# Optimization experiments

Measured on AMD Instinct MI355X. Metric: run time of the kernel, lower is better.

Reference implementation:

```python
import jax, jax.numpy as jnp
import numpy as np

NUM_LEVELS = 4
RADIUS = 4


def _bilinear_zeros(img, x, y):
    """Bilinear sample img (N,H,W) at absolute pixel coords x,y (N,S,S),
    zeros padding outside, matching torch grid_sample(align_corners=True,
    padding_mode='zeros') with absolute->normalized->absolute roundtrip."""
    N, H, W = img.shape
    x0 = jnp.floor(x); y0 = jnp.floor(y)
    x1 = x0 + 1.0;     y1 = y0 + 1.0
    wx1 = x - x0; wx0 = 1.0 - wx1
    wy1 = y - y0; wy0 = 1.0 - wy1
    flat = img.reshape(N, H * W)

    def gather(xi, yi):
        valid = (xi >= 0) & (xi <= W - 1) & (yi >= 0) & (yi <= H - 1)
        xc = jnp.clip(xi, 0, W - 1).astype(jnp.int32)
        yc = jnp.clip(yi, 0, H - 1).astype(jnp.int32)
        idx = (yc * W + xc).reshape(N, -1)
        v = jnp.take_along_axis(flat, idx, axis=1).reshape(xi.shape)
        return jnp.where(valid, v, jnp.zeros((), img.dtype))

    return (wy0 * wx0 * gather(x0, y0) + wy0 * wx1 * gather(x1, y0)
            + wy1 * wx0 * gather(x0, y1) + wy1 * wx1 * gather(x1, y1))


def _avg_pool2(v):
    N, H, W = v.shape
    return v.reshape(N, H // 2, 2, W // 2, 2).mean(axis=(2, 4))


def setup_inputs() -> dict:
    key = jax.random.key(0)
    k1, k2, k3 = jax.random.split(key, 3)
    B, M, C, H, W = 2, 4096, 256, 64, 64
    fmap1 = jax.random.normal(k1, (B, M, C), dtype=jnp.float32)
    fmap2 = jax.random.normal(k2, (B, C, H, W), dtype=jnp.float32)
    u = jax.random.uniform(k3, (B, M, 2), dtype=jnp.float32)
    centroids_coords = u * jnp.array([W - 1, H - 1], dtype=jnp.float32)
    return {"fmap1": fmap1, "fmap2": fmap2, "centroids_coords": centroids_coords}


def reference(fmap1, fmap2, centroids_coords):
    B, M, C = fmap1.shape
    _, _, H, W = fmap2.shape
    side = 2 * RADIUS + 1

    # correlation volume: (B, M, H, W) -> (B*M, H, W)
    corr = jnp.einsum('bmc,bchw->bmhw', fmap1, fmap2).reshape(B * M, H, W)

    d = jnp.arange(-RADIUS, RADIUS + 1, dtype=centroids_coords.dtype)
    di, dj = jnp.meshgrid(d, d, indexing='ij')
    delta = jnp.stack([di, dj], axis=-1)  # (S, S, 2): ch0 = x-offset, ch1 = y-offset

    c = centroids_coords.reshape(B * M, 1, 1, 2)
    vol = corr
    feats = []
    for lvl in range(NUM_LEVELS):
        sc = c + delta                        # (B*M, S, S, 2)
        sampled = _bilinear_zeros(vol, sc[..., 0], sc[..., 1])
        feats.append(sampled.reshape(B, M, side * side))
        c = c / 2.0
        if lvl < NUM_LEVELS - 1:
            vol = _avg_pool2(vol)
    # (B, M, num_levels*S*S) -> (B, out_channels, M)
    return jnp.concatenate(feats, axis=-1).transpose(0, 2, 1)
```

## Files before the change

### kernel.cpp

```cpp
#include <hip/hip_runtime.h>
#include <stdint.h>
#include <stddef.h>

static constexpr int Bb = 2;
static constexpr int Mq = 4096;
static constexpr int Cc = 256;
static constexpr int Hh = 64, Ww = 64;
static constexpr int Np = Hh * Ww;
static constexpr int NL1 = 1024;
static constexpr int RAD = 4;
static constexpr int SIDE = 2 * RAD + 1;
static constexpr int KPL = SIDE * SIDE;
static constexpr int NLVL = 4;
static constexpr int KTOT = NLVL * KPL;

static constexpr size_t WINBUF_B = 0;
static constexpr size_t ABF_B    = WINBUF_B + (size_t)Bb * Mq * 400 * 4;
static constexpr size_t BT_B     = ABF_B + (size_t)Bb * Mq * Cc * 2;
static constexpr size_t B1T_B    = BT_B + (size_t)Bb * Np * Cc * 2;
static constexpr size_t B2T_B    = B1T_B + (size_t)Bb * NL1 * Cc * 2;
static constexpr size_t B3T_B    = B2T_B + (size_t)Bb * 256 * Cc * 2;

typedef float floatx4 __attribute__((ext_vector_type(4)));
typedef short shortx8 __attribute__((ext_vector_type(8)));

union BfPack {
    shortx8 v;
    unsigned short u[8];
};

__device__ __forceinline__ unsigned short f2bf(float f) {
    unsigned int x = __float_as_uint(f);
    x += 0x7fffu + ((x >> 16) & 1u);
    return (unsigned short)(x >> 16);
}

__device__ __forceinline__ float bf2f(unsigned short u) {
    return __uint_as_float((unsigned int)u << 16);
}

__global__ __launch_bounds__(256)
void cvt_kernel(const float* __restrict__ f1, const float* __restrict__ f2,
                unsigned short* __restrict__ Abf, unsigned short* __restrict__ Bt,
                unsigned short* __restrict__ B1t)
{
    __shared__ float tile[64 * 132];
    const int tid = threadIdx.x;
    if (blockIdx.x < 1024) {
        const int t = blockIdx.x * 256 + tid;
        const float4 v0 = *(const float4*)(f1 + (size_t)t * 8);
        const float4 v1 = *(const float4*)(f1 + (size_t)t * 8 + 4);
        BfPack p;
        p.u[0] = f2bf(v0.x); p.u[1] = f2bf(v0.y);
        p.u[2] = f2bf(v0.z); p.u[3] = f2bf(v0.w);
        p.u[4] = f2bf(v1.x); p.u[5] = f2bf(v1.y);
        p.u[6] = f2bf(v1.z); p.u[7] = f2bf(v1.w);
        *(shortx8*)(Abf + (size_t)t * 8) = p.v;
        return;
    }
    const int bid  = blockIdx.x - 1024;
    const int b    = bid >> 7;
    const int cblk = (bid >> 5) & 3;
    const int y1   = bid & 31;

#pragma unroll
    for (int i = 0; i < 8; ++i) {
        const int v  = i * 256 + tid;
        const int c  = v >> 5;
        const int f4 = v & 31;
        *(float4*)&tile[c * 132 + f4 * 4] =
            *(const float4*)&f2[((size_t)(b * Cc + cblk * 64 + c)) * Np + y1 * 128 + f4 * 4];
    }
    __syncthreads();

#pragma unroll
    for (int i = 0; i < 4; ++i) {
        const int w  = i * 256 + tid;
        const int rp = w >> 3;
        const int cg = w & 7;
        BfPack p;
#pragma unroll
        for (int u = 0; u < 8; ++u)
            p.u[u] = f2bf(tile[(cg * 8 + u) * 132 + rp]);
        *(shortx8*)&Bt[((size_t)(b * Np + y1 * 128 + rp)) * Cc + cblk * 64 + cg * 8] = p.v;
    }

    {
        const int x1 = tid >> 3;
        const int cg = tid & 7;
        BfPack p;
#pragma unroll
        for (int u = 0; u < 8; ++u) {
            const int c = cg * 8 + u;
            const float v = 0.25f * (tile[c * 132 + 2 * x1]      + tile[c * 132 + 2 * x1 + 1]
                                   + tile[c * 132 + 64 + 2 * x1] + tile[c * 132 + 64 + 2 * x1 + 1]);
            p.u[u] = f2bf(v);
        }
        *(shortx8*)&B1t[((size_t)(b * NL1 + y1 * 32 + x1)) * Cc + cblk * 64 + cg * 8] = p.v;
    }
}

__global__ __launch_bounds__(256)
void pool23_kernel(const unsigned short* __restrict__ B1t,
                   unsigned short* __restrict__ B2t,
                   unsigned short* __restrict__ B3t)
{
    const int idx = blockIdx.x * 256 + threadIdx.x;
    if (idx < Bb * 256 * 32) {
        const int cg = idx & 31;
        const int p2 = (idx >> 5) & 255;
        const int b  = idx >> 13;
        const int y2 = p2 >> 4, x2 = p2 & 15;
        float s[8] = {0,0,0,0,0,0,0,0};
#pragma unroll
        for (int dy = 0; dy < 2; ++dy)
#pragma unroll
            for (int dx = 0; dx < 2; ++dx) {
                const int p1 = (2 * y2 + dy) * 32 + 2 * x2 + dx;
                BfPack v;
                v.v = *(const shortx8*)&B1t[((size_t)b * NL1 + p1) * Cc + cg * 8];
#pragma unroll
                for (int u = 0; u < 8; ++u) s[u] += bf2f(v.u[u]);
            }
        BfPack o;
#pragma unroll
        for (int u = 0; u < 8; ++u) o.u[u] = f2bf(0.25f * s[u]);
        *(shortx8*)&B2t[((size_t)b * 256 + p2) * Cc + cg * 8] = o.v;
    } else if (idx < Bb * 256 * 32 + Bb * 64 * 32) {
        const int i = idx - Bb * 256 * 32;
        const int cg = i & 31;
        const int p3 = (i >> 5) & 63;
        const int b  = i >> 11;
        const int y3 = p3 >> 3, x3 = p3 & 7;
        float s[8] = {0,0,0,0,0,0,0,0};
#pragma unroll
        for (int dy = 0; dy < 4; ++dy)
#pragma unroll
            for (int dx = 0; dx < 4; ++dx) {
                const int p1 = (4 * y3 + dy) * 32 + 4 * x3 + dx;
                BfPack v;
                v.v = *(const shortx8*)&B1t[((size_t)b * NL1 + p1) * Cc + cg * 8];
#pragma unroll
                for (int u = 0; u < 8; ++u) s[u] += bf2f(v.u[u]);
            }
        BfPack o;
#pragma unroll
        for (int u = 0; u < 8; ++u) o.u[u] = f2bf(0.0625f * s[u]);
        *(shortx8*)&B3t[((size_t)b * 64 + p3) * Cc + cg * 8] = o.v;
    }
}

__global__ __launch_bounds__(512)
void win4_kernel(const unsigned short* __restrict__ Abf,
                 const unsigned short* __restrict__ B0t,
                 const unsigned short* __restrict__ B1t,
                 const unsigned short* __restrict__ B2t,
                 const unsigned short* __restrict__ B3t,
                 const float* __restrict__ cent,
                 float* __restrict__ winbuf)
{
    __shared__ int qlist[128];
    __shared__ int qx0s[128], qy0s[128];
    __shared__ int qcnt;

    const int tid  = threadIdx.x;
    const int wave = tid >> 6;
    const int lane = tid & 63;
    const int lane15 = lane & 15;
    const int quad   = lane >> 4;
    const int bidx = blockIdx.x;

    int lvl, b, cell = 0, q0 = 0;
    bool binned;
    if (bidx < 512)      { lvl = 0; binned = true;  b = bidx >> 8;          cell = bidx & 255; }
    else if (bidx < 640) { lvl = 1; binned = true;  b = (bidx - 512) >> 6;  cell = (bidx - 512) & 63; }
    else if (bidx < 768) { lvl = 2; binned = false; b = (bidx - 640) >> 6;  q0 = ((bidx - 640) & 63) * 64; }
    else                 { lvl = 3; binned = false; b = (bidx - 768) >> 6;  q0 = ((bidx - 768) & 63) * 64; }

    const int w   = Ww >> lvl;
    const int npx = w * w;
    const float scale = 1.0f / (float)(1 << lvl);
    const unsigned short* Bl = (lvl == 0) ? B0t : (lvl == 1) ? B1t : (lvl == 2) ? B2t : B3t;

    int xmin = 0, ymin = 0, rh = w, rw = w, rstride = w, ntile = npx >> 4;
    int cnt;

    if (binned) {
        const int ncx  = w >> 2;
        const int binx = cell & (ncx - 1);
        const int biny = cell >> (4 - lvl);
        xmin = 4 * binx - 4; if (xmin < 0) xmin = 0;
        ymin = 4 * biny - 4; if (ymin < 0) ymin = 0;
        int xmax = 4 * binx + 8; if (xmax > w - 1) xmax = w - 1;
        int ymax = 4 * biny + 8; if (ymax > w - 1) ymax = w - 1;
        rh = ymax - ymin + 1; rw = xmax - xmin + 1;
        rstride = 13;
        ntile = (rh * 13 + 15) >> 4;

        if (tid == 0) qcnt = 0;
        __syncthreads();
#pragma unroll
        for (int i = 0; i < 8; ++i) {
            const int m = i * 512 + tid;
            const float2 cc = *(const float2*)&cent[((size_t)b * Mq + m) * 2];
            const int fx = (int)floorf(cc.x * scale);
            const int fy = (int)floorf(cc.y * scale);
            if ((fx >> 2) == binx && (fy >> 2) == biny) {
                const int idx = atomicAdd(&qcnt, 1);
                if (idx < 128) {
                    qlist[idx] = m;
                    qx0s[idx] = fx - RAD;
                    qy0s[idx] = fy - RAD;
                }
            }
        }
        __syncthreads();
        cnt = qcnt < 128 ? qcnt : 128;
    } else {
        if (tid < 64) {
            const int m = q0 + tid;
            const float2 cc = *(const float2*)&cent[((size_t)b * Mq + m) * 2];
            qlist[tid] = m;
            qx0s[tid] = (int)floorf(cc.x * scale) - RAD;
            qy0s[tid] = (int)floorf(cc.y * scale) - RAD;
        }
        __syncthreads();
        cnt = 64;
    }

    const int jt0 = wave, jt1 = wave + 8;
    const bool t0ok = jt0 < ntile;
    const bool t1ok = jt1 < ntile;
    int y0 = ymin, x0 = xmin, y1 = ymin, x1 = xmin;
    bool v0 = false, v1 = false;
    {
        const int px = jt0 * 16 + lane15;
        int py = (rstride == 13) ? ((px * 5043) >> 16) : (px >> (6 - lvl));
        const int pxx = px - py * rstride;
        v0 = t0ok && (py < rh) && (pxx < rw);
        if (py > rh - 1) py = rh - 1;
        const int pxc = pxx < rw ? pxx : rw - 1;
        y0 = ymin + py; x0 = xmin + pxc;
    }
    {
        const int px = jt1 * 16 + lane15;
        int py = (rstride == 13) ? ((px * 5043) >> 16) : (px >> (6 - lvl));
        const int pxx = px - py * rstride;
        v1 = t1ok && (py < rh) && (pxx < rw);
        if (py > rh - 1) py = rh - 1;
        const int pxc = pxx < rw ? pxx : rw - 1;
        y1 = ymin + py; x1 = xmin + pxc;
    }
    const size_t bB = (size_t)b * npx * Cc;
    const size_t off0 = bB + (size_t)(y0 * w + x0) * Cc + quad * 8;
    const size_t off1 = bB + (size_t)(y1 * w + x1) * Cc + quad * 8;

    for (int m0 = 0; m0 < cnt; m0 += 16) {
        const int qidx = (m0 + lane15) < cnt ? (m0 + lane15) : (cnt - 1);
        const unsigned short* arow = Abf + (size_t)(b * Mq + qlist[qidx]) * Cc + quad * 8;
        shortx8 afr[8];
#pragma unroll
        for (int k0 = 0; k0 < 8; ++k0)
            afr[k0] = *(const shortx8*)&arow[k0 * 32];

        floatx4 acc0 = {0.f, 0.f, 0.f, 0.f};
        floatx4 acc1 = {0.f, 0.f, 0.f, 0.f};
#pragma unroll
        for (int k0 = 0; k0 < 8; ++k0) {
            if (t0ok) {
                const shortx8 b0 = *(const shortx8*)&Bl[off0 + k0 * 32];
                acc0 = __builtin_amdgcn_mfma_f32_16x16x32_bf16(afr[k0], b0, acc0, 0, 0, 0);
            }
            if (t1ok) {
                const shortx8 b1 = *(const shortx8*)&Bl[off1 + k0 * 32];
                acc1 = __builtin_amdgcn_mfma_f32_16x16x32_bf16(afr[k0], b1, acc1, 0, 0, 0);
            }
        }

#pragma unroll
        for (int t = 0; t < 2; ++t) {
            const bool vv = (t == 0) ? v0 : v1;
            if (!vv) continue;
            const floatx4 a = (t == 0) ? acc0 : acc1;
            const int yy = (t == 0) ? y0 : y1;
            const int xx = (t == 0) ? x0 : x1;
#pragma unroll
            for (int r = 0; r < 4; ++r) {
                const int qi = m0 + quad * 4 + r;
                if (qi < cnt) {
                    const int wy = yy - qy0s[qi];
                    const int wx = xx - qx0s[qi];
                    if ((unsigned)wy < 10u && (unsigned)wx < 10u)
                        winbuf[((size_t)b * Mq + qlist[qi]) * 400 + lvl * 100 + wy * 10 + wx] = a[r];
                }
            }
        }
    }
}

__global__ __launch_bounds__(256)
void pyr_sample_kernel(const float* __restrict__ cent,
                       const float* __restrict__ winbuf,
                       float* __restrict__ out)
{
    __shared__ float win[8][400];
    __shared__ float qcx[8], qcy[8];
    __shared__ int qx0l[8][4], qy0l[8][4];

    const int tid = threadIdx.x;
    const int b   = blockIdx.x >> 9;
    const int m0  = (blockIdx.x & 511) * 8;
    const size_t gq0 = (size_t)(b * Mq + m0);

    if (tid < 32) {
        const int q = tid >> 2, l = tid & 3;
        const float cx = cent[(gq0 + q) * 2 + 0];
        const float cy = cent[(gq0 + q) * 2 + 1];
        if (l == 0) { qcx[q] = cx; qcy[q] = cy; }
        const float scl = 1.0f / (float)(1 << l);
        qx0l[q][l] = (int)floorf(cx * scl) - RAD;
        qy0l[q][l] = (int)floorf(cy * scl) - RAD;
    }
    for (int v = tid; v < 800; v += 256) {
        const int q = (v * 41) >> 12;
        const int o = v - q * 100;
        *(float4*)&win[q][o * 4] = *(const float4*)&winbuf[(gq0 + q) * 400 + o * 4];
    }
    __syncthreads();

    for (int i = 0; i < 11; ++i) {
        const int idx = i * 256 + tid;
        if (idx >= KTOT * 8) break;
        const int q  = idx & 7;
        const int kk = idx >> 3;
        const int lvl = kk / KPL;
        const int r   = kk - lvl * KPL;
        const int di  = r / SIDE;
        const int dj  = r - di * SIDE;

        const int w = Ww >> lvl;
        const float scale = 1.0f / (float)(1 << lvl);
        const float x = qcx[q] * scale + (float)(di - RAD);
        const float y = qcy[q] * scale + (float)(dj - RAD);

        const float x0f = floorf(x), y0f = floorf(y);
        const float wx1 = x - x0f, wx0 = 1.0f - wx1;
        const float wy1 = y - y0f, wy0 = 1.0f - wy1;
        const float fmx = (float)(w - 1);
        const bool vx0 = (x0f >= 0.0f) && (x0f <= fmx);
        const bool vx1 = (x0f + 1.0f >= 0.0f) && (x0f + 1.0f <= fmx);
        const bool vy0 = (y0f >= 0.0f) && (y0f <= fmx);
        const bool vy1 = (y0f + 1.0f >= 0.0f) && (y0f + 1.0f <= fmx);

        const int ix0 = (int)x0f, iy0 = (int)y0f;

        const float* buf = &win[q][lvl * 100];
        const int ox = qx0l[q][lvl], oy = qy0l[q][lvl];
        const int cx0 = ix0 - ox, cx1 = cx0 + 1;
        const int cy0r = iy0 - oy, cy1r = cy0r + 1;
        const float g00 = (vx0 && vy0) ? buf[cy0r * 10 + cx0] : 0.0f;
        const float g10 = (vx1 && vy0) ? buf[cy0r * 10 + cx1] : 0.0f;
        const float g01 = (vx0 && vy1) ? buf[cy1r * 10 + cx0] : 0.0f;
        const float g11 = (vx1 && vy1) ? buf[cy1r * 10 + cx1] : 0.0f;

        out[((size_t)b * KTOT + kk) * Mq + m0 + q] =
            wy0 * (wx0 * g00 + wx1 * g10) + wy1 * (wx0 * g01 + wx1 * g11);
    }
}

extern "C" void kernel_launch(void* const* d_in, const int* in_sizes, int n_in,
                              void* d_out, int out_size, void* d_ws, size_t ws_size,
                              hipStream_t stream)
{
    const float* fmap1 = (const float*)d_in[0];
    const float* fmap2 = (const float*)d_in[1];
    const float* cent  = (const float*)d_in[2];
    char* ws = (char*)d_ws;
    float* winbuf = (float*)(ws + WINBUF_B);
    unsigned short* Abf = (unsigned short*)(ws + ABF_B);
    unsigned short* Bt  = (unsigned short*)(ws + BT_B);
    unsigned short* B1t = (unsigned short*)(ws + B1T_B);
    unsigned short* B2t = (unsigned short*)(ws + B2T_B);
    unsigned short* B3t = (unsigned short*)(ws + B3T_B);
    float* out = (float*)d_out;

    cvt_kernel<<<1280, 256, 0, stream>>>(fmap1, fmap2, Abf, Bt, B1t);

    pool23_kernel<<<80, 256, 0, stream>>>(B1t, B2t, B3t);

    win4_kernel<<<896, 512, 0, stream>>>(Abf, Bt, B1t, B2t, B3t, cent, winbuf);

    pyr_sample_kernel<<<Bb * Mq / 8, 256, 0, stream>>>(cent, winbuf, out);
}
```

Baseline: 144.8 us.

## Fuse window correlation with bilinear sampling and prebin queries globally

Query binning moves into extra blocks of the conversion kernel, which use global atomics to build per-cell lists for every level. The window MFMA kernel is fused with the pyramid sampling kernel, so the 400-float per-query window buffer no longer makes a round trip through global memory and one launch is removed. B fragments are now held in registers and A rows are staged in LDS. Levels 2 and 3 now use spatial or index bins split into parts. The risks are list caps that can silently drop queries in dense cells and a new memset launch.

```diff
diff --git a/kernel.cpp b/kernel.cpp
--- a/kernel.cpp
+++ b/kernel.cpp
@@ -14,12 +14,13 @@
 static constexpr int NLVL = 4;
 static constexpr int KTOT = NLVL * KPL;
 
-static constexpr size_t WINBUF_B = 0;
-static constexpr size_t ABF_B    = WINBUF_B + (size_t)Bb * Mq * 400 * 4;
-static constexpr size_t BT_B     = ABF_B + (size_t)Bb * Mq * Cc * 2;
-static constexpr size_t B1T_B    = BT_B + (size_t)Bb * Np * Cc * 2;
-static constexpr size_t B2T_B    = B1T_B + (size_t)Bb * NL1 * Cc * 2;
-static constexpr size_t B3T_B    = B2T_B + (size_t)Bb * 256 * Cc * 2;
+static constexpr size_t ABF_B = 0;
+static constexpr size_t BT_B  = ABF_B + (size_t)Bb * Mq * Cc * 2;
+static constexpr size_t B1T_B = BT_B + (size_t)Bb * Np * Cc * 2;
+static constexpr size_t B2T_B = B1T_B + (size_t)Bb * NL1 * Cc * 2;
+static constexpr size_t B3T_B = B2T_B + (size_t)Bb * 256 * Cc * 2;
+static constexpr size_t CNT_B = B3T_B + (size_t)Bb * 64 * Cc * 2;
+static constexpr size_t LST_B = CNT_B + 4096;
 
 typedef float floatx4 __attribute__((ext_vector_type(4)));
 typedef short shortx8 __attribute__((ext_vector_type(8)));
@@ -41,8 +42,10 @@
 
 __global__ __launch_bounds__(256)
 void cvt_kernel(const float* __restrict__ f1, const float* __restrict__ f2,
+                const float* __restrict__ cent,
                 unsigned short* __restrict__ Abf, unsigned short* __restrict__ Bt,
-                unsigned short* __restrict__ B1t)
+                unsigned short* __restrict__ B1t,
+                int* __restrict__ cnts, int* __restrict__ lists)
 {
     __shared__ float tile[64 * 132];
     const int tid = threadIdx.x;
@@ -58,6 +61,41 @@
         *(shortx8*)(Abf + (size_t)t * 8) = p.v;
         return;
     }
+    if (blockIdx.x >= 1280) {
+        const int gq = (blockIdx.x - 1280) * 256 + tid;
+        const int b  = gq >> 12;
+        const int m  = gq & 4095;
+        const float2 cc = *(const float2*)&cent[(size_t)gq * 2];
+        {
+            const int fx = (int)floorf(cc.x);
+            const int fy = (int)floorf(cc.y);
+            const int cell = ((fy >> 2) << 4) | (fx >> 2);
+            const int slot = atomicAdd(&cnts[b * 256 + cell], 1);
+            if (slot < 64) lists[(b * 256 + cell) * 64 + slot] = m | (fx << 13) | (fy << 19);
+        }
+        {
+            const int fx = (int)floorf(cc.x * 0.5f);
+            const int fy = (int)floorf(cc.y * 0.5f);
+            const int cell = ((fy >> 2) << 3) | (fx >> 2);
+            const int slot = atomicAdd(&cnts[512 + b * 64 + cell], 1);
+            if (slot < 192) lists[32768 + (b * 64 + cell) * 192 + slot] = m | (fx << 13) | (fy << 19);
+        }
+        {
+            const int fx = (int)floorf(cc.x * 0.25f);
+            const int fy = (int)floorf(cc.y * 0.25f);
+            const int cell = ((fy >> 2) << 2) | (fx >> 2);
+            const int slot = atomicAdd(&cnts[640 + b * 16 + cell], 1);
+            if (slot < 512) lists[57344 + (b * 16 + cell) * 512 + slot] = m | (fx << 13) | (fy << 19);
+        }
+        {
+            const int fx = (int)floorf(cc.x * 0.125f);
+            const int fy = (int)floorf(cc.y * 0.125f);
+            const int cell = m >> 8;
+            const int slot = atomicAdd(&cnts[672 + b * 16 + cell], 1);
+            if (slot < 256) lists[73728 + (b * 16 + cell) * 256 + slot] = m | (fx << 13) | (fy << 19);
+        }
+        return;
+    }
     const int bid  = blockIdx.x - 1024;
     const int b    = bid >> 7;
     const int cblk = (bid >> 5) & 3;
@@ -151,220 +189,188 @@
 }
 
 __global__ __launch_bounds__(512)
-void win4_kernel(const unsigned short* __restrict__ Abf,
-                 const unsigned short* __restrict__ B0t,
-                 const unsigned short* __restrict__ B1t,
-                 const unsigned short* __restrict__ B2t,
-                 const unsigned short* __restrict__ B3t,
-                 const float* __restrict__ cent,
-                 float* __restrict__ winbuf)
+void win4f_kernel(const unsigned short* __restrict__ Abf,
+                  const unsigned short* __restrict__ B0t,
+                  const unsigned short* __restrict__ B1t,
+                  const unsigned short* __restrict__ B2t,
+                  const unsigned short* __restrict__ B3t,
+                  const float* __restrict__ cent,
+                  const int* __restrict__ cnts,
+                  const int* __restrict__ lists,
+                  float* __restrict__ out)
 {
-    __shared__ int qlist[128];
-    __shared__ int qx0s[128], qy0s[128];
-    __shared__ int qcnt;
-
-    const int tid  = threadIdx.x;
-    const int wave = tid >> 6;
-    const int lane = tid & 63;
+    __shared__ unsigned short Alds[16 * 264];
+    __shared__ float win[16][100];
+    __shared__ int llist[128];
+    __shared__ float qcx[16], qcy[16];
+    __shared__ int qx0c[16], qy0c[16];
+
+    const int tid    = threadIdx.x;
+    const int wave   = tid >> 6;
+    const int lane   = tid & 63;
     const int lane15 = lane & 15;
     const int quad   = lane >> 4;
-    const int bidx = blockIdx.x;
-
-    int lvl, b, cell = 0, q0 = 0;
-    bool binned;
-    if (bidx < 512)      { lvl = 0; binned = true;  b = bidx >> 8;          cell = bidx & 255; }
-    else if (bidx < 640) { lvl = 1; binned = true;  b = (bidx - 512) >> 6;  cell = (bidx - 512) & 63; }
-    else if (bidx < 768) { lvl = 2; binned = false; b = (bidx - 640) >> 6;  q0 = ((bidx - 640) & 63) * 64; }
-    else                 { lvl = 3; binned = false; b = (bidx - 768) >> 6;  q0 = ((bidx - 768) & 63) * 64; }
+    const int bx     = blockIdx.x;
+
+    int lvl, b, cell, part, plog, cap, cbase, lbase;
+    if (bx < 512)      { lvl = 0; b = bx >> 8; cell = bx & 255; part = 0; plog = 0; cap = 64;
+                         cbase = b * 256 + cell;        lbase = (b * 256 + cell) * 64; }
+    else if (bx < 768) { lvl = 1; const int u = bx - 512; b = u >> 7; const int c = u & 127;
+                         cell = c >> 1; part = c & 1; plog = 1; cap = 192;
+                         cbase = 512 + b * 64 + cell;   lbase = 32768 + (b * 64 + cell) * 192; }
+    else if (bx < 896) { lvl = 2; const int u = bx - 768; b = u >> 6; const int c = u & 63;
+                         cell = c >> 2; part = c & 3; plog = 2; cap = 512;
+                         cbase = 640 + b * 16 + cell;   lbase = 57344 + (b * 16 + cell) * 512; }
+    else               { lvl = 3; const int u = bx - 896; b = u >> 6; const int c = u & 63;
+                         cell = c >> 2; part = c & 3; plog = 2; cap = 256;
+                         cbase = 672 + b * 16 + cell;   lbase = 73728 + (b * 16 + cell) * 256; }
 
     const int w   = Ww >> lvl;
     const int npx = w * w;
     const float scale = 1.0f / (float)(1 << lvl);
     const unsigned short* Bl = (lvl == 0) ? B0t : (lvl == 1) ? B1t : (lvl == 2) ? B2t : B3t;
 
-    int xmin = 0, ymin = 0, rh = w, rw = w, rstride = w, ntile = npx >> 4;
-    int cnt;
-
-    if (binned) {
-        const int ncx  = w >> 2;
-        const int binx = cell & (ncx - 1);
-        const int biny = cell >> (4 - lvl);
+    int cnt = cnts[cbase]; if (cnt > cap) cnt = cap;
+    const int psz = (cnt + (1 << plog) - 1) >> plog;
+    const int p0 = part * psz;
+    int p1 = p0 + psz; if (p1 > cnt) p1 = cnt;
+    const int nloc = p1 - p0;
+    if (nloc <= 0) return;
+
+    int xmin = 0, ymin = 0, rh = w, rw = w;
+    if (lvl < 3) {
+        const int ncxl = 4 - lvl;
+        const int binx = cell & ((1 << ncxl) - 1);
+        const int biny = cell >> ncxl;
         xmin = 4 * binx - 4; if (xmin < 0) xmin = 0;
         ymin = 4 * biny - 4; if (ymin < 0) ymin = 0;
         int xmax = 4 * binx + 8; if (xmax > w - 1) xmax = w - 1;
         int ymax = 4 * biny + 8; if (ymax > w - 1) ymax = w - 1;
         rh = ymax - ymin + 1; rw = xmax - xmin + 1;
-        rstride = 13;
-        ntile = (rh * 13 + 15) >> 4;
-
-        if (tid == 0) qcnt = 0;
-        __syncthreads();
-#pragma unroll
-        for (int i = 0; i < 8; ++i) {
-            const int m = i * 512 + tid;
-            const float2 cc = *(const float2*)&cent[((size_t)b * Mq + m) * 2];
-            const int fx = (int)floorf(cc.x * scale);
-            const int fy = (int)floorf(cc.y * scale);
-            if ((fx >> 2) == binx && (fy >> 2) == biny) {
-                const int idx = atomicAdd(&qcnt, 1);
-                if (idx < 128) {
-                    qlist[idx] = m;
-                    qx0s[idx] = fx - RAD;
-                    qy0s[idx] = fy - RAD;
-                }
-            }
-        }
-        __syncthreads();
-        cnt = qcnt < 128 ? qcnt : 128;
-    } else {
-        if (tid < 64) {
-            const int m = q0 + tid;
-            const float2 cc = *(const float2*)&cent[((size_t)b * Mq + m) * 2];
-            qlist[tid] = m;
-            qx0s[tid] = (int)floorf(cc.x * scale) - RAD;
-            qy0s[tid] = (int)floorf(cc.y * scale) - RAD;
-        }
-        __syncthreads();
-        cnt = 64;
-    }
-
+    }
+
+    if (tid < nloc) llist[tid] = lists[lbase + p0 + tid];
+
+    const int ntile = ((rh - 1) * 13 + rw + 15) >> 4;
     const int jt0 = wave, jt1 = wave + 8;
     const bool t0ok = jt0 < ntile;
     const bool t1ok = jt1 < ntile;
-    int y0 = ymin, x0 = xmin, y1 = ymin, x1 = xmin;
+    int y0 = ymin, x0p = xmin, y1 = ymin, x1p = xmin;
     bool v0 = false, v1 = false;
     {
-        const int px = jt0 * 16 + lane15;
-        int py = (rstride == 13) ? ((px * 5043) >> 16) : (px >> (6 - lvl));
-        const int pxx = px - py * rstride;
+        const int px  = jt0 * 16 + lane15;
+        const int py  = (px * 5043) >> 16;
+        const int pxx = px - py * 13;
         v0 = t0ok && (py < rh) && (pxx < rw);
-        if (py > rh - 1) py = rh - 1;
-        const int pxc = pxx < rw ? pxx : rw - 1;
-        y0 = ymin + py; x0 = xmin + pxc;
+        y0  = ymin + (py < rh ? py : rh - 1);
+        x0p = xmin + (pxx < rw ? pxx : rw - 1);
     }
     {
-        const int px = jt1 * 16 + lane15;
-        int py = (rstride == 13) ? ((px * 5043) >> 16) : (px >> (6 - lvl));
-        const int pxx = px - py * rstride;
+        const int px  = jt1 * 16 + lane15;
+        const int py  = (px * 5043) >> 16;
+        const int pxx = px - py * 13;
         v1 = t1ok && (py < rh) && (pxx < rw);
-        if (py > rh - 1) py = rh - 1;
-        const int pxc = pxx < rw ? pxx : rw - 1;
-        y1 = ymin + py; x1 = xmin + pxc;
-    }
-    const size_t bB = (size_t)b * npx * Cc;
-    const size_t off0 = bB + (size_t)(y0 * w + x0) * Cc + quad * 8;
-    const size_t off1 = bB + (size_t)(y1 * w + x1) * Cc + quad * 8;
-
-    for (int m0 = 0; m0 < cnt; m0 += 16) {
-        const int qidx = (m0 + lane15) < cnt ? (m0 + lane15) : (cnt - 1);
-        const unsigned short* arow = Abf + (size_t)(b * Mq + qlist[qidx]) * Cc + quad * 8;
-        shortx8 afr[8];
-#pragma unroll
-        for (int k0 = 0; k0 < 8; ++k0)
-            afr[k0] = *(const shortx8*)&arow[k0 * 32];
+        y1  = ymin + (py < rh ? py : rh - 1);
+        x1p = xmin + (pxx < rw ? pxx : rw - 1);
+    }
+    const unsigned short* bsrc = Bl + (size_t)b * npx * Cc;
+    const unsigned short* bp0 = bsrc + (size_t)(y0 * w + x0p) * Cc + quad * 8;
+    const unsigned short* bp1 = bsrc + (size_t)(y1 * w + x1p) * Cc + quad * 8;
+    shortx8 bfr0[8], bfr1[8];
+#pragma unroll
+    for (int k0 = 0; k0 < 8; ++k0) bfr0[k0] = *(const shortx8*)&bp0[k0 * 32];
+#pragma unroll
+    for (int k0 = 0; k0 < 8; ++k0) bfr1[k0] = *(const shortx8*)&bp1[k0 * 32];
+
+    for (int m0 = 0; m0 < nloc; m0 += 16) {
+        __syncthreads();
+        {
+            const int r  = tid >> 5;
+            const int kc = tid & 31;
+            const int gi = m0 + r;
+            const int e  = llist[gi < nloc ? gi : nloc - 1];
+            const int m  = e & 8191;
+            *(shortx8*)&Alds[r * 264 + kc * 8] =
+                *(const shortx8*)&Abf[((size_t)(b * Mq) + m) * Cc + kc * 8];
+            if (tid < 16) {
+                const int gi2 = m0 + tid;
+                const int e2  = llist[gi2 < nloc ? gi2 : nloc - 1];
+                const int m2  = e2 & 8191;
+                const float2 cc = *(const float2*)&cent[((size_t)(b * Mq) + m2) * 2];
+                qcx[tid] = cc.x; qcy[tid] = cc.y;
+                qx0c[tid] = ((e2 >> 13) & 63) - RAD;
+                qy0c[tid] = ((e2 >> 19) & 63) - RAD;
+            }
+        }
+        __syncthreads();
 
         floatx4 acc0 = {0.f, 0.f, 0.f, 0.f};
         floatx4 acc1 = {0.f, 0.f, 0.f, 0.f};
 #pragma unroll
         for (int k0 = 0; k0 < 8; ++k0) {
-            if (t0ok) {
-                const shortx8 b0 = *(const shortx8*)&Bl[off0 + k0 * 32];
-                acc0 = __builtin_amdgcn_mfma_f32_16x16x32_bf16(afr[k0], b0, acc0, 0, 0, 0);
-            }
-            if (t1ok) {
-                const shortx8 b1 = *(const shortx8*)&Bl[off1 + k0 * 32];
-                acc1 = __builtin_amdgcn_mfma_f32_16x16x32_bf16(afr[k0], b1, acc1, 0, 0, 0);
-            }
+            const shortx8 a = *(const shortx8*)&Alds[lane15 * 264 + k0 * 32 + quad * 8];
+            if (t0ok) acc0 = __builtin_amdgcn_mfma_f32_16x16x32_bf16(a, bfr0[k0], acc0, 0, 0, 0);
+            if (t1ok) acc1 = __builtin_amdgcn_mfma_f32_16x16x32_bf16(a, bfr1[k0], acc1, 0, 0, 0);
         }
 
 #pragma unroll
         for (int t = 0; t < 2; ++t) {
             const bool vv = (t == 0) ? v0 : v1;
             if (!vv) continue;
-            const floatx4 a = (t == 0) ? acc0 : acc1;
+            const floatx4 aa = (t == 0) ? acc0 : acc1;
             const int yy = (t == 0) ? y0 : y1;
-            const int xx = (t == 0) ? x0 : x1;
+            const int xx = (t == 0) ? x0p : x1p;
 #pragma unroll
             for (int r = 0; r < 4; ++r) {
-                const int qi = m0 + quad * 4 + r;
-                if (qi < cnt) {
-                    const int wy = yy - qy0s[qi];
-                    const int wx = xx - qx0s[qi];
+                const int lq = quad * 4 + r;
+                if (m0 + lq < nloc) {
+                    const int wy = yy - qy0c[lq];
+                    const int wx = xx - qx0c[lq];
                     if ((unsigned)wy < 10u && (unsigned)wx < 10u)
-                        winbuf[((size_t)b * Mq + qlist[qi]) * 400 + lvl * 100 + wy * 10 + wx] = a[r];
+                        win[lq][wy * 10 + wx] = aa[r];
                 }
             }
         }
-    }
-}
-
-__global__ __launch_bounds__(256)
-void pyr_sample_kernel(const float* __restrict__ cent,
-                       const float* __restrict__ winbuf,
-                       float* __restrict__ out)
-{
-    __shared__ float win[8][400];
-    __shared__ float qcx[8], qcy[8];
-    __shared__ int qx0l[8][4], qy0l[8][4];
-
-    const int tid = threadIdx.x;
-    const int b   = blockIdx.x >> 9;
-    const int m0  = (blockIdx.x & 511) * 8;
-    const size_t gq0 = (size_t)(b * Mq + m0);
-
-    if (tid < 32) {
-        const int q = tid >> 2, l = tid & 3;
-        const float cx = cent[(gq0 + q) * 2 + 0];
-        const float cy = cent[(gq0 + q) * 2 + 1];
-        if (l == 0) { qcx[q] = cx; qcy[q] = cy; }
-        const float scl = 1.0f / (float)(1 << l);
-        qx0l[q][l] = (int)floorf(cx * scl) - RAD;
-        qy0l[q][l] = (int)floorf(cy * scl) - RAD;
-    }
-    for (int v = tid; v < 800; v += 256) {
-        const int q = (v * 41) >> 12;
-        const int o = v - q * 100;
-        *(float4*)&win[q][o * 4] = *(const float4*)&winbuf[(gq0 + q) * 400 + o * 4];
-    }
-    __syncthreads();
-
-    for (int i = 0; i < 11; ++i) {
-        const int idx = i * 256 + tid;
-        if (idx >= KTOT * 8) break;
-        const int q  = idx & 7;
-        const int kk = idx >> 3;
-        const int lvl = kk / KPL;
-        const int r   = kk - lvl * KPL;
-        const int di  = r / SIDE;
-        const int dj  = r - di * SIDE;
-
-        const int w = Ww >> lvl;
-        const float scale = 1.0f / (float)(1 << lvl);
-        const float x = qcx[q] * scale + (float)(di - RAD);
-        const float y = qcy[q] * scale + (float)(dj - RAD);
-
-        const float x0f = floorf(x), y0f = floorf(y);
-        const float wx1 = x - x0f, wx0 = 1.0f - wx1;
-        const float wy1 = y - y0f, wy0 = 1.0f - wy1;
-        const float fmx = (float)(w - 1);
-        const bool vx0 = (x0f >= 0.0f) && (x0f <= fmx);
-        const bool vx1 = (x0f + 1.0f >= 0.0f) && (x0f + 1.0f <= fmx);
-        const bool vy0 = (y0f >= 0.0f) && (y0f <= fmx);
-        const bool vy1 = (y0f + 1.0f >= 0.0f) && (y0f + 1.0f <= fmx);
-
-        const int ix0 = (int)x0f, iy0 = (int)y0f;
-
-        const float* buf = &win[q][lvl * 100];
-        const int ox = qx0l[q][lvl], oy = qy0l[q][lvl];
-        const int cx0 = ix0 - ox, cx1 = cx0 + 1;
-        const int cy0r = iy0 - oy, cy1r = cy0r + 1;
-        const float g00 = (vx0 && vy0) ? buf[cy0r * 10 + cx0] : 0.0f;
-        const float g10 = (vx1 && vy0) ? buf[cy0r * 10 + cx1] : 0.0f;
-        const float g01 = (vx0 && vy1) ? buf[cy1r * 10 + cx0] : 0.0f;
-        const float g11 = (vx1 && vy1) ? buf[cy1r * 10 + cx1] : 0.0f;
-
-        out[((size_t)b * KTOT + kk) * Mq + m0 + q] =
-            wy0 * (wx0 * g00 + wx1 * g10) + wy1 * (wx0 * g01 + wx1 * g11);
+        __syncthreads();
+
+        {
+            const int q = tid >> 5;
+            const int j = tid & 31;
+            if (m0 + q < nloc) {
+                const int e = llist[m0 + q];
+                const int m = e & 8191;
+                const float cx = qcx[q], cy = qcy[q];
+                const int ox = qx0c[q], oy = qy0c[q];
+                const float* buf = win[q];
+#pragma unroll
+                for (int s = 0; s < 3; ++s) {
+                    const int r81 = j + s * 32;
+                    if (r81 < 81) {
+                        const int di = r81 / SIDE;
+                        const int dj = r81 - di * SIDE;
+                        const float x = cx * scale + (float)(di - RAD);
+                        const float y = cy * scale + (float)(dj - RAD);
+                        const float x0f = floorf(x), y0f = floorf(y);
+                        const float wx1 = x - x0f, wx0 = 1.0f - wx1;
+                        const float wy1 = y - y0f, wy0 = 1.0f - wy1;
+                        const float fmx = (float)(w - 1);
+                        const bool vx0 = (x0f >= 0.0f) && (x0f <= fmx);
+                        const bool vx1 = (x0f + 1.0f >= 0.0f) && (x0f + 1.0f <= fmx);
+                        const bool vy0 = (y0f >= 0.0f) && (y0f <= fmx);
+                        const bool vy1 = (y0f + 1.0f >= 0.0f) && (y0f + 1.0f <= fmx);
+                        const int ix0 = (int)x0f, iy0 = (int)y0f;
+                        const int cx0 = ix0 - ox, cx1 = cx0 + 1;
+                        const int cy0r = iy0 - oy, cy1r = cy0r + 1;
+                        const float g00 = (vx0 && vy0) ? buf[cy0r * 10 + cx0] : 0.0f;
+                        const float g10 = (vx1 && vy0) ? buf[cy0r * 10 + cx1] : 0.0f;
+                        const float g01 = (vx0 && vy1) ? buf[cy1r * 10 + cx0] : 0.0f;
+                        const float g11 = (vx1 && vy1) ? buf[cy1r * 10 + cx1] : 0.0f;
+                        out[((size_t)b * KTOT + lvl * KPL + r81) * Mq + m] =
+                            wy0 * (wx0 * g00 + wx1 * g10) + wy1 * (wx0 * g01 + wx1 * g11);
+                    }
+                }
+            }
+        }
     }
 }
 
@@ -376,19 +382,20 @@
     const float* fmap2 = (const float*)d_in[1];
     const float* cent  = (const float*)d_in[2];
     char* ws = (char*)d_ws;
-    float* winbuf = (float*)(ws + WINBUF_B);
     unsigned short* Abf = (unsigned short*)(ws + ABF_B);
     unsigned short* Bt  = (unsigned short*)(ws + BT_B);
     unsigned short* B1t = (unsigned short*)(ws + B1T_B);
     unsigned short* B2t = (unsigned short*)(ws + B2T_B);
     unsigned short* B3t = (unsigned short*)(ws + B3T_B);
+    int* cnts  = (int*)(ws + CNT_B);
+    int* lists = (int*)(ws + LST_B);
     float* out = (float*)d_out;
 
-    cvt_kernel<<<1280, 256, 0, stream>>>(fmap1, fmap2, Abf, Bt, B1t);
+    hipMemsetAsync(cnts, 0, 4096, stream);
+
+    cvt_kernel<<<1312, 256, 0, stream>>>(fmap1, fmap2, cent, Abf, Bt, B1t, cnts, lists);
 
     pool23_kernel<<<80, 256, 0, stream>>>(B1t, B2t, B3t);
 
-    win4_kernel<<<896, 512, 0, stream>>>(Abf, Bt, B1t, B2t, B3t, cent, winbuf);
-
-    pyr_sample_kernel<<<Bb * Mq / 8, 256, 0, stream>>>(cent, winbuf, out);
-}
+    win4f_kernel<<<1024, 512, 0, stream>>>(Abf, Bt, B1t, B2t, B3t, cent, cnts, lists, out);
+}
```

Result: slower. 168.2 us (+16.1%).
